# Kernel tuning notes

Hardware: AMD Instinct MI355X
Metric: run time of the kernel (lower is better)

Reference implementation:

```python
import jax, jax.numpy as jnp
import numpy as np

LAMBDA_INIT = 0.8


def setup_inputs() -> dict:
    key = jax.random.key(0)
    ks = jax.random.split(key, 12)
    B, T, E = 2, 2048, 1024
    H = 8            # num_heads // 2 diff-heads
    HS = 64          # head_size
    DO = 128         # 2 * head_output_dimension (per-head output dim)
    q = jax.random.normal(ks[0], (B, T, E), jnp.float32)
    k = jax.random.normal(ks[1], (B, T, E), jnp.float32)
    v = jax.random.normal(ks[2], (B, T, E), jnp.float32)
    s = E ** -0.5  # linear-layer style init scale
    Wq = jax.random.normal(ks[3], (H, E, 2 * HS), jnp.float32) * s
    Wk = jax.random.normal(ks[4], (H, E, 2 * HS), jnp.float32) * s
    Wv = jax.random.normal(ks[5], (H, E, DO), jnp.float32) * s
    # lambda reparam vectors (scaled 0.1 to keep exp(dot) numerically tame)
    lq1 = jax.random.normal(ks[6], (H, HS), jnp.float32) * 0.1
    lk1 = jax.random.normal(ks[7], (H, HS), jnp.float32) * 0.1
    lq2 = jax.random.normal(ks[8], (H, HS), jnp.float32) * 0.1
    lk2 = jax.random.normal(ks[9], (H, HS), jnp.float32) * 0.1
    Wp = jax.random.normal(ks[10], (H * DO, E), jnp.float32) * (H * DO) ** -0.5
    bp = jnp.zeros((E,), jnp.float32)
    # buffer: tril(ones, diagonal=1); positions where it is 0 get -inf
    mask = jnp.tril(jnp.ones((T, T), jnp.bool_), 1)
    return {"q": q, "k": k, "v": v, "Wq": Wq, "Wk": Wk, "Wv": Wv,
            "lq1": lq1, "lk1": lk1, "lq2": lq2, "lk2": lk2,
            "Wp": Wp, "bp": bp, "mask": mask}


def reference(q, k, v, Wq, Wk, Wv, lq1, lk1, lq2, lk2, Wp, bp, mask):
    B, T, E = q.shape
    H = Wq.shape[0]
    HS = Wq.shape[-1] // 2
    scale = HS ** -0.5
    Q = jnp.einsum('bte,hed->bhtd', q, Wq)   # [B,H,T,2HS]
    K = jnp.einsum('bte,hed->bhtd', k, Wk)
    V = jnp.einsum('bte,hed->bhtd', v, Wv)   # [B,H,T,DO]
    Q1, Q2 = jnp.split(Q, 2, axis=-1)
    K1, K2 = jnp.split(K, 2, axis=-1)
    neg_inf = jnp.float32(-jnp.inf)
    s1 = jnp.einsum('bhtd,bhsd->bhts', Q1, K1) * scale
    s2 = jnp.einsum('bhtd,bhsd->bhts', Q2, K2) * scale
    s1 = jnp.where(mask[:T, :T], s1, neg_inf)
    s2 = jnp.where(mask[:T, :T], s2, neg_inf)
    a1 = jax.nn.softmax(s1, axis=-1)
    a2 = jax.nn.softmax(s2, axis=-1)
    lbd = (jnp.exp(jnp.sum(lq1 * lk1, -1)) - jnp.exp(jnp.sum(lq2 * lk2, -1))
           + LAMBDA_INIT)                     # [H]
    attn = a1 - lbd[None, :, None, None] * a2
    ctx = jnp.einsum('bhts,bhsd->bhtd', attn, V) * (1.0 - LAMBDA_INIT)
    out = ctx.transpose(0, 2, 1, 3).reshape(B, T, -1)  # concat heads
    return out @ Wp + bp
```

## Files before the change

### kernel.cpp

```cpp
#include <hip/hip_runtime.h>
#include <hip/hip_bf16.h>


constexpr int Tn = 2048;
constexpr int En = 1024;
constexpr int Hn = 8;
constexpr float LAMBDA_INIT = 0.8f;
constexpr float QSCALE = 0.18033688011112042f;
constexpr size_t SZb = (size_t)2 * Tn * En;
constexpr size_t WSZ = (size_t)En * En;

typedef __attribute__((ext_vector_type(8))) short short8;
typedef __attribute__((ext_vector_type(4))) short s16x4;
typedef __attribute__((ext_vector_type(4))) float f32x4;

__device__ __forceinline__ short f2bf(float x) {
  union { __hip_bfloat16 h; short s; } u;
  u.h = __float2bfloat16(x);
  return u.s;
}
__device__ __forceinline__ void gload16(const short* g, short* l) {
  __builtin_amdgcn_global_load_lds(
      (const __attribute__((address_space(1))) void*)g,
      (__attribute__((address_space(3))) void*)l, 16, 0, 0);
}

__global__ __launch_bounds__(256)
void cvt3(const float* __restrict__ q, const float* __restrict__ k,
          const float* __restrict__ v, short* __restrict__ ws) {
  const float* src = (blockIdx.y == 0) ? q : (blockIdx.y == 1) ? k : v;
  short* dst = ws + (size_t)blockIdx.y * SZb;
  const size_t i = ((size_t)blockIdx.x * 256 + threadIdx.x) * 8;
  float4 a = *(const float4*)&src[i];
  float4 b = *(const float4*)&src[i + 4];
  short8 o;
  o[0] = f2bf(a.x); o[1] = f2bf(a.y); o[2] = f2bf(a.z); o[3] = f2bf(a.w);
  o[4] = f2bf(b.x); o[5] = f2bf(b.y); o[6] = f2bf(b.z); o[7] = f2bf(b.w);
  *(short8*)&dst[i] = o;
}

__global__ __launch_bounds__(256)
void twt(const float* __restrict__ Wq, const float* __restrict__ Wk,
         const float* __restrict__ Wv, const float* __restrict__ Wp,
         short* __restrict__ WT) {
  __shared__ float tl[64][65];
  const int id = blockIdx.x;
  const int tid = threadIdx.x;
  const float* src;
  short* dst;
  int r0, c0, C;
  if (id < 768) {
    const int wi = id >> 8;
    const float* W = (wi == 0) ? Wq : (wi == 1) ? Wk : Wv;
    const int rem = id & 255;
    const int h = rem >> 5;
    const int tile = rem & 31;
    r0 = (tile >> 1) * 64;
    c0 = (tile & 1) * 64;
    C = 128;
    src = W + (size_t)h * En * 128;
    dst = WT + (size_t)wi * WSZ + (size_t)h * 128 * En;
  } else {
    const int idx = id - 768;
    r0 = (idx >> 4) * 64;
    c0 = (idx & 15) * 64;
    C = En;
    src = Wp;
    dst = WT + 3 * WSZ;
  }
  const int r = tid >> 2, cc = (tid & 3) * 16;
#pragma unroll
  for (int j = 0; j < 4; ++j) {
    const float4 x = *(const float4*)&src[(size_t)(r0 + r) * C + c0 + cc + j * 4];
    tl[r][cc + j * 4 + 0] = x.x;
    tl[r][cc + j * 4 + 1] = x.y;
    tl[r][cc + j * 4 + 2] = x.z;
    tl[r][cc + j * 4 + 3] = x.w;
  }
  __syncthreads();
  const int c = tid >> 2, rc = (tid & 3) * 16;
  short8 o0, o1;
#pragma unroll
  for (int e = 0; e < 8; ++e) {
    o0[e] = f2bf(tl[rc + e][c]);
    o1[e] = f2bf(tl[rc + 8 + e][c]);
  }
  *(short8*)&dst[(size_t)(c0 + c) * En + r0 + rc] = o0;
  *(short8*)&dst[(size_t)(c0 + c) * En + r0 + rc + 8] = o1;
}

__global__ __launch_bounds__(256)
void qkv_mfma2(const short* __restrict__ Xq, const short* __restrict__ Xk,
               const short* __restrict__ Xv, const short* __restrict__ WT,
               short* __restrict__ Qo, short* __restrict__ Ko,
               short* __restrict__ Vto) {
  __shared__ __align__(16) short As[2][4096];
  __shared__ __align__(16) short Bs2[2][4096];
  const int which = blockIdx.z;
  const short* X = (which == 0) ? Xq : (which == 1) ? Xk : Xv;
  const int head = blockIdx.y;
  const int m0 = blockIdx.x * 128;
  const short* Bt = WT + (size_t)which * WSZ + (size_t)head * 128 * En;
  const float oscale = (which == 0) ? QSCALE : 1.0f;

  const int tid = threadIdx.x;
  const int lane = tid & 63;
  const int w = tid >> 6, wr = w >> 1, wc = w & 1;
  const int fr = lane & 15, fk = (lane >> 4) * 8;
  const int srow = tid >> 2, sch = (tid & 3) * 8;
  const int wdst = w * 512;

#define QSTAGE(BUF, K0)                                                  \
  {                                                                      \
    _Pragma("unroll") for (int j = 0; j < 2; ++j) {                      \
      gload16(&X[(size_t)(m0 + j * 64 + srow) * En + (K0) + sch],        \
              &As[BUF][j * 2048 + wdst]);                                \
      gload16(&Bt[(size_t)(j * 64 + srow) * En + (K0) + sch],            \
              &Bs2[BUF][j * 2048 + wdst]);                               \
    }                                                                    \
  }

  f32x4 acc[4][4] = {};
  QSTAGE(0, 0);
  for (int k0 = 0; k0 < En; k0 += 32) {
    const int cur = (k0 >> 5) & 1;
    if (k0 + 32 < En) {
      QSTAGE(cur ^ 1, k0 + 32);
      __builtin_amdgcn_sched_barrier(0);
      asm volatile("s_waitcnt vmcnt(4)" ::: "memory");
      __builtin_amdgcn_sched_barrier(0);
    } else {
      __builtin_amdgcn_sched_barrier(0);
      asm volatile("s_waitcnt vmcnt(0)" ::: "memory");
      __builtin_amdgcn_sched_barrier(0);
    }
    __builtin_amdgcn_s_barrier();

    short8 a[4], b[4];
#pragma unroll
    for (int i = 0; i < 4; ++i)
      a[i] = *(const short8*)&As[cur][(wr * 64 + i * 16 + fr) * 32 + fk];
#pragma unroll
    for (int j = 0; j < 4; ++j)
      b[j] = *(const short8*)&Bs2[cur][(wc * 64 + j * 16 + fr) * 32 + fk];
#pragma unroll
    for (int i = 0; i < 4; ++i)
#pragma unroll
      for (int j = 0; j < 4; ++j)
        acc[i][j] = __builtin_amdgcn_mfma_f32_16x16x32_bf16(a[i], b[j],
                                                            acc[i][j], 0, 0, 0);
    __builtin_amdgcn_s_barrier();
  }
#undef QSTAGE

  const int crow = (lane >> 4) * 4, ccol = lane & 15;
  if (which == 2) {
#pragma unroll
    for (int i = 0; i < 4; ++i) {
      const int m = m0 + wr * 64 + i * 16 + crow;
      const int bb = m >> 11, t = m & (Tn - 1);
#pragma unroll
      for (int j = 0; j < 4; ++j) {
        const int d = wc * 64 + j * 16 + ccol;
        s16x4 pk;
#pragma unroll
        for (int p = 0; p < 4; ++p) pk[p] = f2bf(acc[i][j][p]);
        *(s16x4*)&Vto[((size_t)(bb * Hn + head) * 128 + d) * Tn + t] = pk;
      }
    }
  } else {
    short* Out = (which == 0) ? Qo : Ko;
#pragma unroll
    for (int i = 0; i < 4; ++i) {
      const int m = m0 + wr * 64 + i * 16 + crow;
      const int bb = m >> 11, t = m & (Tn - 1);
      short* dst = Out + ((size_t)(bb * Hn + head) * Tn + t) * 128;
#pragma unroll
      for (int j = 0; j < 4; ++j) {
        const int d = wc * 64 + j * 16 + ccol;
#pragma unroll
        for (int p = 0; p < 4; ++p)
          dst[(size_t)p * 128 + d] = f2bf(acc[i][j][p] * oscale);
      }
    }
  }
}

__global__ __launch_bounds__(256)
void proj_mfma2(const short* __restrict__ Xb, const short* __restrict__ WpT,
                const float* __restrict__ bias, float* __restrict__ Out) {
  __shared__ __align__(16) short As[2][2048];
  __shared__ __align__(16) short Bs2[2][4096];
  const int m0 = blockIdx.x * 64;
  const int n0 = blockIdx.y * 128;

  const int tid = threadIdx.x;
  const int lane = tid & 63;
  const int w = tid >> 6, wr = w >> 1, wc = w & 1;
  const int fr = lane & 15, fk = (lane >> 4) * 8;
  const int srow = tid >> 2, sch = (tid & 3) * 8;
  const int wdst = w * 512;

#define PSTAGE(BUF, K0)                                                  \
  {                                                                      \
    gload16(&Xb[(size_t)(m0 + srow) * En + (K0) + sch],                  \
            &As[BUF][wdst]);                                             \
    _Pragma("unroll") for (int j = 0; j < 2; ++j)                        \
      gload16(&WpT[(size_t)(n0 + j * 64 + srow) * En + (K0) + sch],      \
              &Bs2[BUF][j * 2048 + wdst]);                               \
  }

  f32x4 acc[2][4] = {};
  PSTAGE(0, 0);
  for (int k0 = 0; k0 < En; k0 += 32) {
    const int cur = (k0 >> 5) & 1;
    if (k0 + 32 < En) {
      PSTAGE(cur ^ 1, k0 + 32);
      __builtin_amdgcn_sched_barrier(0);
      asm volatile("s_waitcnt vmcnt(3)" ::: "memory");
      __builtin_amdgcn_sched_barrier(0);
    } else {
      __builtin_amdgcn_sched_barrier(0);
      asm volatile("s_waitcnt vmcnt(0)" ::: "memory");
      __builtin_amdgcn_sched_barrier(0);
    }
    __builtin_amdgcn_s_barrier();

    short8 a[2], b[4];
#pragma unroll
    for (int i = 0; i < 2; ++i)
      a[i] = *(const short8*)&As[cur][(wr * 32 + i * 16 + fr) * 32 + fk];
#pragma unroll
    for (int j = 0; j < 4; ++j)
      b[j] = *(const short8*)&Bs2[cur][(wc * 64 + j * 16 + fr) * 32 + fk];
#pragma unroll
    for (int i = 0; i < 2; ++i)
#pragma unroll
      for (int j = 0; j < 4; ++j)
        acc[i][j] = __builtin_amdgcn_mfma_f32_16x16x32_bf16(a[i], b[j],
                                                            acc[i][j], 0, 0, 0);
    __builtin_amdgcn_s_barrier();
  }
#undef PSTAGE

  const int crow = (lane >> 4) * 4, ccol = lane & 15;
#pragma unroll
  for (int i = 0; i < 2; ++i) {
    const int m = m0 + wr * 32 + i * 16 + crow;
#pragma unroll
    for (int j = 0; j < 4; ++j) {
      const int n = n0 + wc * 64 + j * 16 + ccol;
      const float bv = bias[n];
#pragma unroll
      for (int p = 0; p < 4; ++p)
        Out[(size_t)(m + p) * En + n] = acc[i][j][p] + bv;
    }
  }
}

__global__ __launch_bounds__(256, 4)
void diff_attn7(const short* __restrict__ Qg, const short* __restrict__ Kg,
                const short* __restrict__ Vtg,
                const float* __restrict__ lq1, const float* __restrict__ lk1,
                const float* __restrict__ lq2, const float* __restrict__ lk2,
                short* __restrict__ ctxb) {
  __shared__ __align__(16) short pool[18688];

  const int lin = blockIdx.x;
  const int h = lin & 7;
  const int idx = lin >> 3;
  const int b = idx >> 5;
  const int x = idx & 31;
  const int tid = threadIdx.x;
  const int lane = tid & 63;
  const int w = tid >> 6;
  const int st = w >> 1, wh = w & 1;
  const int fr = lane & 15, hi = lane >> 4;
  const int swz = fr & 7;
  const int swv = (fr ^ (fr >> 2)) & 3;
  const size_t basebh = (size_t)(b * Hn + h) * Tn * 128;

  float lbd;
  {
    float a1 = lq1[h * 64 + lane] * lk1[h * 64 + lane];
    float a2 = lq2[h * 64 + lane] * lk2[h * 64 + lane];
#pragma unroll
    for (int off = 1; off <= 32; off <<= 1) {
      a1 += __shfl_xor(a1, off);
      a2 += __shfl_xor(a2, off);
    }
    lbd = __expf(a1) - __expf(a2) + LAMBDA_INIT;
  }

  int ksrc[2], vsrc[2], dsto[2];
#pragma unroll
  for (int j = 0; j < 2; ++j) {
    const int ob = j * 4096 + tid * 16;
    { const int s = ob >> 8, cp = (ob >> 4) & 15, c = cp ^ (s & 7);
      ksrc[j] = s * 128 + c * 8; }
    { const int d = ob >> 6, cp = (ob >> 4) & 3,
          c = cp ^ ((d ^ (d >> 2)) & 3);
      vsrc[j] = d * Tn + c * 8; }
    dsto[j] = (j * 4096 + w * 1024) >> 1;
  }
  const short* kgb = Kg + basebh;
  const short* vgb = Vtg + basebh;

#define STAGE(BUF, S0)                                                   \
  {                                                                      \
    const short* kb_ = kgb + (size_t)(S0) * 128;                         \
    const short* vb_ = vgb + (S0);                                       \
    _Pragma("unroll") for (int j = 0; j < 2; ++j) {                      \
      gload16(kb_ + ksrc[j], pool + (BUF) * 4096 + dsto[j]);             \
      gload16(vb_ + vsrc[j], pool + 8192 + (BUF) * 4096 + dsto[j]);      \
    }                                                                    \
  }

  short8 ones;
#pragma unroll
  for (int e = 0; e < 8; ++e) ones[e] = (short)0x3F80;
  short* Plw = pool + 16384 + w * 576;

  auto phase = [&](int qi) {
    const int q0 = qi * 32;
    const int NT = min(Tn / 32, qi + 2);
    const int tmin = q0 + wh * 16;
    const int tbase = tmin + hi * 4;

    short8 qf[2];
    {
      const short* qp = Qg + basebh + (size_t)(tmin + fr) * 128 + st * 64;
      qf[0] = *(const short8*)(qp + hi * 8);
      qf[1] = *(const short8*)(qp + 32 + hi * 8);
    }
    f32x4 o[8] = {};
    f32x4 ol = {};

    STAGE(0, 0);
    int cur = 0;
    for (int t = 0; t < NT; ++t) {
      const int s0 = t * 32;
      if (t + 1 < NT) {
        STAGE(cur ^ 1, s0 + 32);
        __builtin_amdgcn_sched_barrier(0);
        asm volatile("s_waitcnt vmcnt(4)" ::: "memory");
        __builtin_amdgcn_sched_barrier(0);
      } else {
        __builtin_amdgcn_sched_barrier(0);
        asm volatile("s_waitcnt vmcnt(0)" ::: "memory");
        __builtin_amdgcn_sched_barrier(0);
      }
      __builtin_amdgcn_s_barrier();

      if (s0 <= tmin + 16) {
        const short* Kb = pool + cur * 4096;
        const short* Vb = pool + 8192 + cur * 4096;
        const bool interior = (tmin - s0) >= 30;

        f32x4 s4[2] = {};
        __builtin_amdgcn_s_setprio(1);
#pragma unroll
        for (int sb = 0; sb < 2; ++sb) {
          const int rb = (sb * 16 + fr) * 128;
#pragma unroll
          for (int kp = 0; kp < 2; ++kp) {
            const short8 kb = *(const short8*)
                &Kb[rb + ((st * 8 + ((kp * 4 + hi) ^ swz)) << 3)];
            s4[sb] = __builtin_amdgcn_mfma_f32_16x16x32_bf16(qf[kp], kb,
                                                             s4[sb], 0, 0, 0);
          }
        }
        __builtin_amdgcn_s_setprio(0);
        if (!interior) {
#pragma unroll
          for (int sb = 0; sb < 2; ++sb) {
            const int sg = s0 + sb * 16 + fr;
#pragma unroll
            for (int p = 0; p < 4; ++p)
              if (sg > tbase + p + 1) s4[sb][p] = -1e30f;
          }
        }

#pragma unroll
        for (int sb = 0; sb < 2; ++sb)
#pragma unroll
          for (int p = 0; p < 4; ++p)
            Plw[(hi * 4 + p) * 36 + sb * 16 + fr] =
                f2bf(exp2f(s4[sb][p] - 12.0f));

        const short8 pf = *(const short8*)&Plw[fr * 36 + hi * 8];
        __builtin_amdgcn_s_setprio(1);
        ol = __builtin_amdgcn_mfma_f32_16x16x32_bf16(ones, pf, ol, 0, 0, 0);
#pragma unroll
        for (int dblk = 0; dblk < 8; ++dblk) {
          const short8 va = *(const short8*)
              &Vb[(dblk * 16 + fr) * 32 + ((hi ^ swv) << 3)];
          o[dblk] = __builtin_amdgcn_mfma_f32_16x16x32_bf16(va, pf, o[dblk],
                                                            0, 0, 0);
        }
        __builtin_amdgcn_s_setprio(0);
      }

      __builtin_amdgcn_s_barrier();
      cur ^= 1;
    }

    const float lr = ol[0];
    float* O2L = (float*)pool;
    if (st == 1) {
      const float c2 = (1.0f - LAMBDA_INIT) * lbd / lr;
#pragma unroll
      for (int dblk = 0; dblk < 8; ++dblk)
#pragma unroll
        for (int e = 0; e < 4; ++e)
          O2L[wh * 2176 + (dblk * 16 + hi * 4 + e) * 17 + fr] =
              c2 * o[dblk][e];
    }
    __syncthreads();
    if (st == 0) {
      const float c1 = (1.0f - LAMBDA_INIT) / lr;
      const int t = tmin + fr;
      short* dst = ctxb + ((size_t)b * Tn + t) * En + h * 128;
#pragma unroll
      for (int dblk = 0; dblk < 8; ++dblk) {
        s16x4 pk;
#pragma unroll
        for (int e = 0; e < 4; ++e)
          pk[e] = f2bf(c1 * o[dblk][e] -
                       O2L[wh * 2176 + (dblk * 16 + hi * 4 + e) * 17 + fr]);
        *(s16x4*)&dst[dblk * 16 + hi * 4] = pk;
      }
    }
    __syncthreads();
  };

  phase(63 - x);
  phase(x);
#undef STAGE
}

extern "C" void kernel_launch(void* const* d_in, const int* in_sizes, int n_in,
                              void* d_out, int out_size, void* d_ws, size_t ws_size,
                              hipStream_t stream) {
  const float* q   = (const float*)d_in[0];
  const float* k   = (const float*)d_in[1];
  const float* v   = (const float*)d_in[2];
  const float* Wq  = (const float*)d_in[3];
  const float* Wk  = (const float*)d_in[4];
  const float* Wv  = (const float*)d_in[5];
  const float* lq1 = (const float*)d_in[6];
  const float* lk1 = (const float*)d_in[7];
  const float* lq2 = (const float*)d_in[8];
  const float* lk2 = (const float*)d_in[9];
  const float* Wp  = (const float*)d_in[10];
  const float* bp  = (const float*)d_in[11];

  short* ws = (short*)d_ws;
  short* qbf = ws;
  short* kbf = ws + SZb;
  short* vbf = ws + 2 * SZb;
  short* Qb  = ws + 3 * SZb;
  short* Kb  = ws + 4 * SZb;
  short* Vtb = ws + 5 * SZb;
  short* WT  = ws + 6 * SZb;
  short* ctxb = qbf;

  cvt3<<<dim3(2048, 3), dim3(256), 0, stream>>>(q, k, v, ws);
  twt<<<dim3(1024), dim3(256), 0, stream>>>(Wq, Wk, Wv, Wp, WT);
  qkv_mfma2<<<dim3(32, 8, 3), dim3(256), 0, stream>>>(qbf, kbf, vbf, WT,
                                                      Qb, Kb, Vtb);
  diff_attn7<<<dim3(512), dim3(256), 0, stream>>>(Qb, Kb, Vtb,
                                                  lq1, lk1, lq2, lk2, ctxb);
  proj_mfma2<<<dim3(64, 8), dim3(256), 0, stream>>>(ctxb, WT + 3 * WSZ, bp,
                                                    (float*)d_out);
}
```

Baseline: 143.7 us.

## Split attention tile across eight waves by key half and output-dim half

```diff
diff --git a/kernel.cpp b/kernel.cpp
--- a/kernel.cpp
+++ b/kernel.cpp
@@ -258,12 +258,12 @@
   }
 }
 
-__global__ __launch_bounds__(256, 4)
-void diff_attn7(const short* __restrict__ Qg, const short* __restrict__ Kg,
-                const short* __restrict__ Vtg,
-                const float* __restrict__ lq1, const float* __restrict__ lk1,
-                const float* __restrict__ lq2, const float* __restrict__ lk2,
-                short* __restrict__ ctxb) {
+__global__ __launch_bounds__(512, 4)
+void diff_attn10(const short* __restrict__ Qg, const short* __restrict__ Kg,
+                 const short* __restrict__ Vtg,
+                 const float* __restrict__ lq1, const float* __restrict__ lk1,
+                 const float* __restrict__ lq2, const float* __restrict__ lk2,
+                 short* __restrict__ ctxb) {
   __shared__ __align__(16) short pool[18688];
 
   const int lin = blockIdx.x;
@@ -274,7 +274,7 @@
   const int tid = threadIdx.x;
   const int lane = tid & 63;
   const int w = tid >> 6;
-  const int st = w >> 1, wh = w & 1;
+  const int st = w >> 2, wh = (w >> 1) & 1, kh = w & 1;
   const int fr = lane & 15, hi = lane >> 4;
   const int swz = fr & 7;
   const int swv = (fr ^ (fr >> 2)) & 3;
@@ -292,34 +292,29 @@
     lbd = __expf(a1) - __expf(a2) + LAMBDA_INIT;
   }
 
-  int ksrc[2], vsrc[2], dsto[2];
-#pragma unroll
-  for (int j = 0; j < 2; ++j) {
-    const int ob = j * 4096 + tid * 16;
+  int ksrc, vsrc;
+  {
+    const int ob = tid * 16;
     { const int s = ob >> 8, cp = (ob >> 4) & 15, c = cp ^ (s & 7);
-      ksrc[j] = s * 128 + c * 8; }
+      ksrc = s * 128 + c * 8; }
     { const int d = ob >> 6, cp = (ob >> 4) & 3,
           c = cp ^ ((d ^ (d >> 2)) & 3);
-      vsrc[j] = d * Tn + c * 8; }
-    dsto[j] = (j * 4096 + w * 1024) >> 1;
-  }
+      vsrc = d * Tn + c * 8; }
+  }
+  const int dsto = w * 512;
   const short* kgb = Kg + basebh;
   const short* vgb = Vtg + basebh;
 
 #define STAGE(BUF, S0)                                                   \
   {                                                                      \
-    const short* kb_ = kgb + (size_t)(S0) * 128;                         \
-    const short* vb_ = vgb + (S0);                                       \
-    _Pragma("unroll") for (int j = 0; j < 2; ++j) {                      \
-      gload16(kb_ + ksrc[j], pool + (BUF) * 4096 + dsto[j]);             \
-      gload16(vb_ + vsrc[j], pool + 8192 + (BUF) * 4096 + dsto[j]);      \
-    }                                                                    \
+    gload16(kgb + (size_t)(S0) * 128 + ksrc, pool + (BUF) * 4096 + dsto);\
+    gload16(vgb + (S0) + vsrc, pool + 8192 + (BUF) * 4096 + dsto);       \
   }
 
   short8 ones;
 #pragma unroll
   for (int e = 0; e < 8; ++e) ones[e] = (short)0x3F80;
-  short* Plw = pool + 16384 + w * 576;
+  short* Plw = pool + 16384 + (st * 2 + wh) * 576;
 
   auto phase = [&](int qi) {
     const int q0 = qi * 32;
@@ -333,7 +328,7 @@
       qf[0] = *(const short8*)(qp + hi * 8);
       qf[1] = *(const short8*)(qp + 32 + hi * 8);
     }
-    f32x4 o[8] = {};
+    f32x4 o[4] = {};
     f32x4 ol = {};
 
     STAGE(0, 0);
@@ -343,7 +338,7 @@
       if (t + 1 < NT) {
         STAGE(cur ^ 1, s0 + 32);
         __builtin_amdgcn_sched_barrier(0);
-        asm volatile("s_waitcnt vmcnt(4)" ::: "memory");
+        asm volatile("s_waitcnt vmcnt(2)" ::: "memory");
         __builtin_amdgcn_sched_barrier(0);
       } else {
         __builtin_amdgcn_sched_barrier(0);
@@ -352,51 +347,51 @@
       }
       __builtin_amdgcn_s_barrier();
 
-      if (s0 <= tmin + 16) {
-        const short* Kb = pool + cur * 4096;
-        const short* Vb = pool + 8192 + cur * 4096;
+      const bool active = (s0 <= tmin + 16);
+      const short* Kb = pool + cur * 4096;
+      const short* Vb = pool + 8192 + cur * 4096;
+
+      if (active) {
         const bool interior = (tmin - s0) >= 30;
-
-        f32x4 s4[2] = {};
+        f32x4 s4 = {};
+        const int rb = (kh * 16 + fr) * 128;
         __builtin_amdgcn_s_setprio(1);
 #pragma unroll
-        for (int sb = 0; sb < 2; ++sb) {
-          const int rb = (sb * 16 + fr) * 128;
-#pragma unroll
-          for (int kp = 0; kp < 2; ++kp) {
-            const short8 kb = *(const short8*)
-                &Kb[rb + ((st * 8 + ((kp * 4 + hi) ^ swz)) << 3)];
-            s4[sb] = __builtin_amdgcn_mfma_f32_16x16x32_bf16(qf[kp], kb,
-                                                             s4[sb], 0, 0, 0);
-          }
+        for (int kp = 0; kp < 2; ++kp) {
+          const short8 kb = *(const short8*)
+              &Kb[rb + ((st * 8 + ((kp * 4 + hi) ^ swz)) << 3)];
+          s4 = __builtin_amdgcn_mfma_f32_16x16x32_bf16(qf[kp], kb,
+                                                       s4, 0, 0, 0);
         }
         __builtin_amdgcn_s_setprio(0);
         if (!interior) {
-#pragma unroll
-          for (int sb = 0; sb < 2; ++sb) {
-            const int sg = s0 + sb * 16 + fr;
-#pragma unroll
-            for (int p = 0; p < 4; ++p)
-              if (sg > tbase + p + 1) s4[sb][p] = -1e30f;
-          }
+          const int sg = s0 + kh * 16 + fr;
+#pragma unroll
+          for (int p = 0; p < 4; ++p)
+            if (sg > tbase + p + 1) s4[p] = -1e30f;
         }
-
-#pragma unroll
-        for (int sb = 0; sb < 2; ++sb)
-#pragma unroll
-          for (int p = 0; p < 4; ++p)
-            Plw[(hi * 4 + p) * 36 + sb * 16 + fr] =
-                f2bf(exp2f(s4[sb][p] - 12.0f));
-
+#pragma unroll
+        for (int p = 0; p < 4; ++p)
+          Plw[(hi * 4 + p) * 36 + kh * 16 + fr] =
+              f2bf(exp2f(s4[p] - 12.0f));
+      }
+
+      __builtin_amdgcn_sched_barrier(0);
+      asm volatile("s_waitcnt lgkmcnt(0)" ::: "memory");
+      __builtin_amdgcn_sched_barrier(0);
+      __builtin_amdgcn_s_barrier();
+
+      if (active) {
         const short8 pf = *(const short8*)&Plw[fr * 36 + hi * 8];
         __builtin_amdgcn_s_setprio(1);
         ol = __builtin_amdgcn_mfma_f32_16x16x32_bf16(ones, pf, ol, 0, 0, 0);
 #pragma unroll
-        for (int dblk = 0; dblk < 8; ++dblk) {
+        for (int j = 0; j < 4; ++j) {
+          const int dblk = kh * 4 + j;
           const short8 va = *(const short8*)
               &Vb[(dblk * 16 + fr) * 32 + ((hi ^ swv) << 3)];
-          o[dblk] = __builtin_amdgcn_mfma_f32_16x16x32_bf16(va, pf, o[dblk],
-                                                            0, 0, 0);
+          o[j] = __builtin_amdgcn_mfma_f32_16x16x32_bf16(va, pf, o[j],
+                                                         0, 0, 0);
         }
         __builtin_amdgcn_s_setprio(0);
       }
@@ -410,11 +405,13 @@
     if (st == 1) {
       const float c2 = (1.0f - LAMBDA_INIT) * lbd / lr;
 #pragma unroll
-      for (int dblk = 0; dblk < 8; ++dblk)
+      for (int j = 0; j < 4; ++j) {
+        const int dblk = kh * 4 + j;
 #pragma unroll
         for (int e = 0; e < 4; ++e)
           O2L[wh * 2176 + (dblk * 16 + hi * 4 + e) * 17 + fr] =
-              c2 * o[dblk][e];
+              c2 * o[j][e];
+      }
     }
     __syncthreads();
     if (st == 0) {
@@ -422,11 +419,12 @@
       const int t = tmin + fr;
       short* dst = ctxb + ((size_t)b * Tn + t) * En + h * 128;
 #pragma unroll
-      for (int dblk = 0; dblk < 8; ++dblk) {
+      for (int j = 0; j < 4; ++j) {
+        const int dblk = kh * 4 + j;
         s16x4 pk;
 #pragma unroll
         for (int e = 0; e < 4; ++e)
-          pk[e] = f2bf(c1 * o[dblk][e] -
+          pk[e] = f2bf(c1 * o[j][e] -
                        O2L[wh * 2176 + (dblk * 16 + hi * 4 + e) * 17 + fr]);
         *(s16x4*)&dst[dblk * 16 + hi * 4] = pk;
       }
@@ -469,8 +467,8 @@
   twt<<<dim3(1024), dim3(256), 0, stream>>>(Wq, Wk, Wv, Wp, WT);
   qkv_mfma2<<<dim3(32, 8, 3), dim3(256), 0, stream>>>(qbf, kbf, vbf, WT,
                                                       Qb, Kb, Vtb);
-  diff_attn7<<<dim3(512), dim3(256), 0, stream>>>(Qb, Kb, Vtb,
-                                                  lq1, lk1, lq2, lk2, ctxb);
+  diff_attn10<<<dim3(512), dim3(512), 0, stream>>>(Qb, Kb, Vtb,
+                                                   lq1, lk1, lq2, lk2, ctxb);
   proj_mfma2<<<dim3(64, 8), dim3(256), 0, stream>>>(ctxb, WT + 3 * WSZ, bp,
                                                     (float*)d_out);
 }
```

New measurement: 156.1 us. 1.09x slower.
